# Kernel tuning notes

Measured on AMD Instinct MI355X. Metric: run time of the kernel, lower is better.

The kernel has to match this reference:

```python
import jax, jax.numpy as jnp
import numpy as np

IN_DIM = 512
OUT_DIM = 512
DEGREE = 3
KNOTS = (0.2, 0.4, 0.6, 0.8)
SDIM = DEGREE + 1 + len(KNOTS)  # 8
BATCH = 2048


def truncated_power_basis(t):
    # t: (B,) -> (B, SDIM)
    cols = [jnp.ones_like(t)]
    for p in range(1, DEGREE + 1):
        cols.append(t ** p)
    for c in KNOTS:  # degree > 1 branch: relu(t - knot)^degree
        cols.append(jax.nn.relu(t - c) ** DEGREE)
    return jnp.stack(cols, axis=1)


def setup_inputs() -> dict:
    key = jax.random.key(0)
    k0, k1, k2 = jax.random.split(key, 3)
    inputs = jax.random.uniform(k0, (BATCH, IN_DIM + 1), dtype=jnp.float32)
    # xavier_uniform for W_wts (fan_in=SDIM, fan_out=IN_DIM*OUT_DIM)
    limW = float(np.sqrt(6.0 / (SDIM + IN_DIM * OUT_DIM)))
    W_wts = jax.random.uniform(k1, (SDIM, IN_DIM * OUT_DIM), dtype=jnp.float32,
                               minval=-limW, maxval=limW)
    limb = float(np.sqrt(6.0 / (SDIM + OUT_DIM)))
    b_wts = jax.random.uniform(k2, (SDIM, OUT_DIM), dtype=jnp.float32,
                               minval=-limb, maxval=limb)
    return {"inputs": inputs, "W_wts": W_wts, "b_wts": b_wts}


def reference(inputs, W_wts, b_wts):
    treatment = inputs[:, 0]          # (B,)
    features = inputs[:, 1:]          # (B, IN_DIM)
    basis = truncated_power_basis(treatment)  # (B, SDIM)
    Wk = W_wts.reshape(SDIM, IN_DIM, OUT_DIM)
    # fused: per-sample weight W[b] = sum_s basis[b,s] * Wk[s]; out[b] = features[b] @ W[b]
    out = jnp.einsum('bs,bi,sio->bo', basis, features, Wk)
    out = out + basis @ b_wts         # (B, OUT_DIM)
    return out
```

## Files before the change

### kernel.cpp

```cpp
#include <hip/hip_runtime.h>
#include <stdint.h>

#define BATCH   2048
#define INDIM   512
#define OUTDIM  512
#define KP      4352
#define NBLK_A  2048
#define NBLK_B  544
#define SPLITK  4
#define KSTEPS  17

typedef __attribute__((ext_vector_type(4))) float  f32x4;
typedef __attribute__((ext_vector_type(8))) __bf16 bf16x8;
typedef __attribute__((ext_vector_type(8))) unsigned short u16x8;
typedef __attribute__((ext_vector_type(4))) unsigned short u16x4;

__device__ __forceinline__ unsigned short f2bf(float x) {
  unsigned int u = __float_as_uint(x);
  u += 0x7fffu + ((u >> 16) & 1u);
  return (unsigned short)(u >> 16);
}

__device__ __forceinline__ void llds16(const void* g, void* s) {
  __builtin_amdgcn_global_load_lds(
      (__attribute__((address_space(1))) void*)g,
      (__attribute__((address_space(3))) void*)s, 16, 0, 0);
}

__global__ __launch_bounds__(256) void prep_kernel(
    const float* __restrict__ inp, const float* __restrict__ W,
    const float* __restrict__ bwts, unsigned short* __restrict__ Abf,
    unsigned short* __restrict__ Btf) {
  const int tid = threadIdx.x;
  const int bx  = blockIdx.x;
  if (bx < NBLK_A) {
    const float* row = inp + (size_t)bx * (INDIM + 1);
    const float t = row[0];
    float bs[8];
    bs[0] = 1.0f; bs[1] = t; bs[2] = t * t; bs[3] = bs[2] * t;
    const float kn[4] = {0.2f, 0.4f, 0.6f, 0.8f};
#pragma unroll
    for (int c = 0; c < 4; ++c) {
      float d = fmaxf(t - kn[c], 0.0f);
      bs[4 + c] = d * d * d;
    }
    unsigned short* Arow = Abf + (size_t)bx * KP;
    for (int k4 = tid * 4; k4 < KP; k4 += 1024) {
      float v0, v1, v2, v3;
      if (k4 < 4096) {
        const float s = bs[k4 >> 9];
        const int i = k4 & 511;
        v0 = s * row[1 + i]; v1 = s * row[2 + i];
        v2 = s * row[3 + i]; v3 = s * row[4 + i];
      } else if (k4 < 4104) {
        const int s0 = k4 - 4096;
        v0 = bs[s0]; v1 = bs[s0 + 1]; v2 = bs[s0 + 2]; v3 = bs[s0 + 3];
      } else {
        v0 = v1 = v2 = v3 = 0.0f;
      }
      u16x4 o;
      o.x = f2bf(v0); o.y = f2bf(v1); o.z = f2bf(v2); o.w = f2bf(v3);
      *(u16x4*)&Arow[k4] = o;
    }
  } else {
    const int bb = bx - NBLK_A;
    const int kt = bb >> 3, ntile = bb & 7;
    const int k0 = kt * 64, n0 = ntile * 64;
    __shared__ float Ts[64][65];
#pragma unroll
    for (int p = 0; p < 4; ++p) {
      const int r  = (tid >> 4) + p * 16;
      const int c4 = (tid & 15) * 4;
      const int k  = k0 + r;
      float4 v;
      if (k < 4096)      v = *(const float4*)&W[(size_t)k * 512 + n0 + c4];
      else if (k < 4104) v = *(const float4*)&bwts[(size_t)(k - 4096) * 512 + n0 + c4];
      else               v = make_float4(0.f, 0.f, 0.f, 0.f);
      Ts[c4 + 0][r] = v.x; Ts[c4 + 1][r] = v.y;
      Ts[c4 + 2][r] = v.z; Ts[c4 + 3][r] = v.w;
    }
    __syncthreads();
    const int nl  = tid >> 2;
    const int kcc = (tid & 3) * 16;
    u16x8 o0, o1;
#pragma unroll
    for (int q = 0; q < 8; ++q) {
      o0[q] = f2bf(Ts[nl][kcc + q]);
      o1[q] = f2bf(Ts[nl][kcc + 8 + q]);
    }
    unsigned short* dst = Btf + (size_t)(n0 + nl) * KP + k0 + kcc;
    *(u16x8*)dst = o0;
    *(u16x8*)(dst + 8) = o1;
  }
}

__global__ __launch_bounds__(256, 4) void gemm_kernel(
    const unsigned short* __restrict__ Abf,
    const unsigned short* __restrict__ Btf,
    float* __restrict__ out) {
  const int tid  = threadIdx.x;
  const int kc   = blockIdx.x & (SPLITK - 1);
  const int tile = blockIdx.x >> 2;
  const int nt = tile & 7, mt = tile >> 3;
  const int m0 = mt * 64, n0 = nt * 64;
  const int l = tid & 63, w = tid >> 6;
  const int wm = w >> 1, wn = w & 1;
  const int quad = l >> 4, lr = l & 15;

  __shared__ __align__(16) unsigned short As[64 * 64];
  __shared__ __align__(16) unsigned short Bs[64 * 64];

  f32x4 acc00 = {}, acc01 = {}, acc10 = {}, acc11 = {};

  const int sr = tid >> 3, pc = tid & 7;
  const int lc = pc ^ (sr & 7);
  const unsigned short* Ag = Abf + (size_t)(m0 + sr) * KP + lc * 8;
  const unsigned short* Bg = Btf + (size_t)(n0 + sr) * KP + lc * 8;
  unsigned short* AsW = &As[sr * 64 + pc * 8];
  unsigned short* BsW = &Bs[sr * 64 + pc * 8];

  const int sx  = lr & 7;
  const int ar  = (wm * 32 + lr) * 64;
  const int br  = (wn * 32 + lr) * 64;
  const int c0  = ((0 + quad) ^ sx) * 8;
  const int c1  = ((4 + quad) ^ sx) * 8;

  int koff = kc * (KSTEPS * 64);
  for (int it = 0; it < KSTEPS; ++it) {
    llds16(Ag + koff,           AsW);
    llds16(Ag + koff + 32 * KP, AsW + 32 * 64);
    llds16(Bg + koff,           BsW);
    llds16(Bg + koff + 32 * KP, BsW + 32 * 64);
    __syncthreads();

    bf16x8 a00 = *(const bf16x8*)&As[ar + c0];
    bf16x8 a10 = *(const bf16x8*)&As[ar + 1024 + c0];
    bf16x8 b00 = *(const bf16x8*)&Bs[br + c0];
    bf16x8 b10 = *(const bf16x8*)&Bs[br + 1024 + c0];
    bf16x8 a01 = *(const bf16x8*)&As[ar + c1];
    bf16x8 a11 = *(const bf16x8*)&As[ar + 1024 + c1];
    bf16x8 b01 = *(const bf16x8*)&Bs[br + c1];
    bf16x8 b11 = *(const bf16x8*)&Bs[br + 1024 + c1];

    acc00 = __builtin_amdgcn_mfma_f32_16x16x32_bf16(a00, b00, acc00, 0, 0, 0);
    acc01 = __builtin_amdgcn_mfma_f32_16x16x32_bf16(a00, b10, acc01, 0, 0, 0);
    acc10 = __builtin_amdgcn_mfma_f32_16x16x32_bf16(a10, b00, acc10, 0, 0, 0);
    acc11 = __builtin_amdgcn_mfma_f32_16x16x32_bf16(a10, b10, acc11, 0, 0, 0);
    acc00 = __builtin_amdgcn_mfma_f32_16x16x32_bf16(a01, b01, acc00, 0, 0, 0);
    acc01 = __builtin_amdgcn_mfma_f32_16x16x32_bf16(a01, b11, acc01, 0, 0, 0);
    acc10 = __builtin_amdgcn_mfma_f32_16x16x32_bf16(a11, b01, acc10, 0, 0, 0);
    acc11 = __builtin_amdgcn_mfma_f32_16x16x32_bf16(a11, b11, acc11, 0, 0, 0);

    __syncthreads();
    koff += 64;
  }

  const int col = n0 + wn * 32 + lr;
  const int row = m0 + wm * 32 + quad * 4;
  float* o00 = out + (size_t)row * OUTDIM + col;
#pragma unroll
  for (int r = 0; r < 4; ++r) {
    unsafeAtomicAdd(o00 + (size_t)r * OUTDIM,             acc00[r]);
    unsafeAtomicAdd(o00 + (size_t)r * OUTDIM + 16,        acc01[r]);
    unsafeAtomicAdd(o00 + (size_t)(16 + r) * OUTDIM,      acc10[r]);
    unsafeAtomicAdd(o00 + (size_t)(16 + r) * OUTDIM + 16, acc11[r]);
  }
}

extern "C" void kernel_launch(void* const* d_in, const int* in_sizes, int n_in,
                              void* d_out, int out_size, void* d_ws, size_t ws_size,
                              hipStream_t stream) {
  const float* inp  = (const float*)d_in[0];
  const float* W    = (const float*)d_in[1];
  const float* bwts = (const float*)d_in[2];
  float* out = (float*)d_out;

  unsigned short* Abf = (unsigned short*)d_ws;
  unsigned short* Btf = Abf + (size_t)BATCH * KP;

  hipMemsetAsync(d_out, 0, (size_t)BATCH * OUTDIM * sizeof(float), stream);
  prep_kernel<<<NBLK_A + NBLK_B, 256, 0, stream>>>(inp, W, bwts, Abf, Btf);
  gemm_kernel<<<(BATCH / 64) * (OUTDIM / 64) * SPLITK, 256, 0, stream>>>(Abf, Btf, out);
}
```

Baseline: 100.4 us.

## Compute bias term in prep kernel, drop memset and K padding, remap blocks to XCDs

The bias contribution basis @ b_wts is now computed in fp32 directly in the prep kernel, which also initialises the output, so the separate memset and the padded K tail (4352 to 4096) go away. This trims the GEMM by one K step per split and shrinks the bf16 staging buffers. The GEMM block index is also remapped so that blocks sharing an XCD work on related tiles, aiming for better L2 locality. The bias now stays fp32 instead of bf16, and correctness relies on prep_kernel writing out before the gemm atomics run.

```diff
diff --git a/kernel.cpp b/kernel.cpp
--- a/kernel.cpp
+++ b/kernel.cpp
@@ -4,11 +4,11 @@
 #define BATCH   2048
 #define INDIM   512
 #define OUTDIM  512
-#define KP      4352
+#define KTOT    4096
 #define NBLK_A  2048
-#define NBLK_B  544
+#define NBLK_B  512
 #define SPLITK  4
-#define KSTEPS  17
+#define KSTEPS  16
 
 typedef __attribute__((ext_vector_type(4))) float  f32x4;
 typedef __attribute__((ext_vector_type(8))) __bf16 bf16x8;
@@ -30,7 +30,7 @@
 __global__ __launch_bounds__(256) void prep_kernel(
     const float* __restrict__ inp, const float* __restrict__ W,
     const float* __restrict__ bwts, unsigned short* __restrict__ Abf,
-    unsigned short* __restrict__ Btf) {
+    unsigned short* __restrict__ Btf, float* __restrict__ out) {
   const int tid = threadIdx.x;
   const int bx  = blockIdx.x;
   if (bx < NBLK_A) {
@@ -44,23 +44,25 @@
       float d = fmaxf(t - kn[c], 0.0f);
       bs[4 + c] = d * d * d;
     }
-    unsigned short* Arow = Abf + (size_t)bx * KP;
-    for (int k4 = tid * 4; k4 < KP; k4 += 1024) {
-      float v0, v1, v2, v3;
-      if (k4 < 4096) {
-        const float s = bs[k4 >> 9];
-        const int i = k4 & 511;
-        v0 = s * row[1 + i]; v1 = s * row[2 + i];
-        v2 = s * row[3 + i]; v3 = s * row[4 + i];
-      } else if (k4 < 4104) {
-        const int s0 = k4 - 4096;
-        v0 = bs[s0]; v1 = bs[s0 + 1]; v2 = bs[s0 + 2]; v3 = bs[s0 + 3];
-      } else {
-        v0 = v1 = v2 = v3 = 0.0f;
-      }
+    unsigned short* Arow = Abf + (size_t)bx * KTOT;
+#pragma unroll
+    for (int it = 0; it < 4; ++it) {
+      const int k4 = tid * 4 + it * 1024;
+      const float s = bs[k4 >> 9];
+      const int i = k4 & 511;
       u16x4 o;
-      o.x = f2bf(v0); o.y = f2bf(v1); o.z = f2bf(v2); o.w = f2bf(v3);
+      o.x = f2bf(s * row[1 + i]); o.y = f2bf(s * row[2 + i]);
+      o.z = f2bf(s * row[3 + i]); o.w = f2bf(s * row[4 + i]);
       *(u16x4*)&Arow[k4] = o;
+    }
+    float* orow = out + (size_t)bx * OUTDIM;
+#pragma unroll
+    for (int rep = 0; rep < 2; ++rep) {
+      const int o = tid + rep * 256;
+      float acc = 0.f;
+#pragma unroll
+      for (int s = 0; s < 8; ++s) acc += bs[s] * bwts[s * OUTDIM + o];
+      orow[o] = acc;
     }
   } else {
     const int bb = bx - NBLK_A;
@@ -71,11 +73,7 @@
     for (int p = 0; p < 4; ++p) {
       const int r  = (tid >> 4) + p * 16;
       const int c4 = (tid & 15) * 4;
-      const int k  = k0 + r;
-      float4 v;
-      if (k < 4096)      v = *(const float4*)&W[(size_t)k * 512 + n0 + c4];
-      else if (k < 4104) v = *(const float4*)&bwts[(size_t)(k - 4096) * 512 + n0 + c4];
-      else               v = make_float4(0.f, 0.f, 0.f, 0.f);
+      float4 v = *(const float4*)&W[(size_t)(k0 + r) * 512 + n0 + c4];
       Ts[c4 + 0][r] = v.x; Ts[c4 + 1][r] = v.y;
       Ts[c4 + 2][r] = v.z; Ts[c4 + 3][r] = v.w;
     }
@@ -88,7 +86,7 @@
       o0[q] = f2bf(Ts[nl][kcc + q]);
       o1[q] = f2bf(Ts[nl][kcc + 8 + q]);
     }
-    unsigned short* dst = Btf + (size_t)(n0 + nl) * KP + k0 + kcc;
+    unsigned short* dst = Btf + (size_t)(n0 + nl) * KTOT + k0 + kcc;
     *(u16x8*)dst = o0;
     *(u16x8*)(dst + 8) = o1;
   }
@@ -99,9 +97,12 @@
     const unsigned short* __restrict__ Btf,
     float* __restrict__ out) {
   const int tid  = threadIdx.x;
-  const int kc   = blockIdx.x & (SPLITK - 1);
-  const int tile = blockIdx.x >> 2;
-  const int nt = tile & 7, mt = tile >> 3;
+  const int xcd  = blockIdx.x & 7;
+  const int slot = blockIdx.x >> 3;
+  const int kc    = xcd & 3;
+  const int mhalf = xcd >> 2;
+  const int nt    = slot & 7;
+  const int mt    = mhalf * 16 + (slot >> 3);
   const int m0 = mt * 64, n0 = nt * 64;
   const int l = tid & 63, w = tid >> 6;
   const int wm = w >> 1, wn = w & 1;
@@ -114,8 +115,8 @@
 
   const int sr = tid >> 3, pc = tid & 7;
   const int lc = pc ^ (sr & 7);
-  const unsigned short* Ag = Abf + (size_t)(m0 + sr) * KP + lc * 8;
-  const unsigned short* Bg = Btf + (size_t)(n0 + sr) * KP + lc * 8;
+  const unsigned short* Ag = Abf + (size_t)(m0 + sr) * KTOT + lc * 8;
+  const unsigned short* Bg = Btf + (size_t)(n0 + sr) * KTOT + lc * 8;
   unsigned short* AsW = &As[sr * 64 + pc * 8];
   unsigned short* BsW = &Bs[sr * 64 + pc * 8];
 
@@ -127,10 +128,10 @@
 
   int koff = kc * (KSTEPS * 64);
   for (int it = 0; it < KSTEPS; ++it) {
-    llds16(Ag + koff,           AsW);
-    llds16(Ag + koff + 32 * KP, AsW + 32 * 64);
-    llds16(Bg + koff,           BsW);
-    llds16(Bg + koff + 32 * KP, BsW + 32 * 64);
+    llds16(Ag + koff,            AsW);
+    llds16(Ag + koff + 32 * KTOT, AsW + 32 * 64);
+    llds16(Bg + koff,            BsW);
+    llds16(Bg + koff + 32 * KTOT, BsW + 32 * 64);
     __syncthreads();
 
     bf16x8 a00 = *(const bf16x8*)&As[ar + c0];
@@ -176,9 +177,8 @@
   float* out = (float*)d_out;
 
   unsigned short* Abf = (unsigned short*)d_ws;
-  unsigned short* Btf = Abf + (size_t)BATCH * KP;
+  unsigned short* Btf = Abf + (size_t)BATCH * KTOT;
 
-  hipMemsetAsync(d_out, 0, (size_t)BATCH * OUTDIM * sizeof(float), stream);
-  prep_kernel<<<NBLK_A + NBLK_B, 256, 0, stream>>>(inp, W, bwts, Abf, Btf);
+  prep_kernel<<<NBLK_A + NBLK_B, 256, 0, stream>>>(inp, W, bwts, Abf, Btf, out);
   gemm_kernel<<<(BATCH / 64) * (OUTDIM / 64) * SPLITK, 256, 0, stream>>>(Abf, Btf, out);
 }
```

After: 100.7 us. About the same (+0.3%).
